# Kernel tuning notes

Hardware: AMD Instinct MI355X
Metric: run time of the kernel (lower is better)

Reference implementation:

```python
import jax, jax.numpy as jnp
import numpy as np

N_FREQS = 8
ALPHA = 16.0
SCALING = ALPHA / N_FREQS  # alpha / n_freqs
EPS = 1e-8


def setup_inputs() -> dict:
    key = jax.random.key(0)
    ks = jax.random.split(key, 6)
    B, S, IN, OUT = 4, 2048, 4096, 4096
    x = jax.random.normal(ks[0], (B, S, IN), dtype=jnp.float32)
    W = jax.random.normal(ks[1], (OUT, IN), dtype=jnp.float32) * 0.02
    bias = jax.random.normal(ks[2], (OUT,), dtype=jnp.float32) * 0.02
    delta_real = jax.random.normal(ks[3], (N_FREQS, N_FREQS), dtype=jnp.float32)
    delta_imag = jax.random.normal(ks[4], (N_FREQS, N_FREQS), dtype=jnp.float32)
    # m is initialized in torch as row-norm of the base weight; emulate that here
    m = jnp.linalg.norm(W, axis=1, keepdims=True)
    return {"x": x, "W": W, "bias": bias,
            "delta_real": delta_real, "delta_imag": delta_imag, "m": m}


def _dora_weight(W, delta_real, delta_imag, m):
    # full-size rfft2 of the frozen base weight (norm='ortho')
    W_fft = jnp.fft.rfft2(W, norm="ortho")            # [OUT, IN//2+1] complex
    fh, fw = delta_real.shape                          # freq_h, freq_w (low-freq corner)
    delta = jax.lax.complex(delta_real, delta_imag) * SCALING
    W_fft = W_fft.at[:fh, :fw].add(delta)              # pad-to-full + add, fused
    W_mod = jnp.fft.irfft2(W_fft, s=W.shape, norm="ortho")  # [OUT, IN] real
    # DoRA: magnitude m times unit row-direction
    norm = jnp.linalg.norm(W_mod, axis=1, keepdims=True)     # [OUT, 1]
    return m * W_mod / (norm + EPS)


def reference(x, W, bias, delta_real, delta_imag, m):
    W_dora = _dora_weight(W, delta_real, delta_imag, m)      # [OUT, IN]
    # F.linear: x @ W^T + b
    return jnp.einsum("bsi,oi->bso", x, W_dora) + bias
```

## Files before the change

### kernel.cpp

```cpp
#include <hip/hip_runtime.h>
#include <hip/hip_bf16.h>

typedef __attribute__((ext_vector_type(4))) float f32x4;
typedef __attribute__((ext_vector_type(8))) short bf16x8;

#define IN_DIM 4096
#define OUT_DIM 4096
#define MROWS 8192
#define NFREQ 8
#define TWO_PI 6.283185307179586f

#define BK 64
#define NT (IN_DIM / BK)
#define LDS_BUF 32768
#define LDS_HALF 16384
#define LDS_B_REGION 65536

__device__ __forceinline__ unsigned int f2bf(float f) {
    union { float f; unsigned int u; } a;
    a.f = f;
    unsigned int u = a.u;
    u += 0x7fffu + ((u >> 16) & 1u);
    return u >> 16;
}

#define ROT_C 0.9999988234517019f
#define ROT_S 0.0015339801862847655f

__global__ __launch_bounds__(256) void prep_kernel(
    const float* __restrict__ x,
    const float* __restrict__ W,
    const float* __restrict__ dre,
    const float* __restrict__ dimg,
    const float* __restrict__ mrow,
    unsigned short* __restrict__ Wd,
    unsigned short* __restrict__ xb)
{
    const int t = threadIdx.x;

    if (blockIdx.x >= OUT_DIM) {
        const size_t idx = (size_t)(blockIdx.x - OUT_DIM) * 256 + t;
        const f32x4* p = (const f32x4*)(x + idx * 8);
        const f32x4 a = p[0], b = p[1];
        uint4 o;
        o.x = f2bf(a[0]) | (f2bf(a[1]) << 16);
        o.y = f2bf(a[2]) | (f2bf(a[3]) << 16);
        o.z = f2bf(b[0]) | (f2bf(b[1]) << 16);
        o.w = f2bf(b[2]) | (f2bf(b[3]) << 16);
        *(uint4*)(xb + idx * 8) = o;
        return;
    }

    const int o = blockIdx.x;

    float P[NFREQ], Q[NFREQ];
#pragma unroll
    for (int w = 0; w < NFREQ; ++w) { P[w] = 0.f; Q[w] = 0.f; }
#pragma unroll
    for (int h = 0; h < NFREQ; ++h) {
        const float th = (TWO_PI / 4096.0f) * (float)((h * o) & 4095);
        const float sh = __sinf(th), ch = __cosf(th);
#pragma unroll
        for (int w = 0; w < NFREQ; ++w) {
            const float A = 2.0f * dre[h * NFREQ + w];
            const float B = 2.0f * dimg[h * NFREQ + w];
            P[w] += A * ch - B * sh;
            Q[w] += A * sh + B * ch;
        }
    }
#pragma unroll
    for (int w = 0; w < NFREQ; ++w) {
        const float c = (w == 0 ? 1.0f : 2.0f) * (1.0f / 4096.0f);
        P[w] *= c; Q[w] *= c;
    }

    const int i0 = t * 16;
    const f32x4* wrow = (const f32x4*)(W + (size_t)o * IN_DIM + i0);
    float vals[16];
    float ss = 0.0f;

    const float beta0 = (TWO_PI / 4096.0f) * (float)i0;
    float cb = __cosf(beta0), sb = __sinf(beta0);

#pragma unroll
    for (int q = 0; q < 4; ++q) {
        const f32x4 wv = wrow[q];
#pragma unroll
        for (int j = 0; j < 4; ++j) {
            float cw = cb, sw = sb;
            float d = P[0] + P[1] * cw - Q[1] * sw;
#pragma unroll
            for (int w = 2; w < NFREQ; ++w) {
                const float cn = cw * cb - sw * sb;
                sw = sw * cb + cw * sb;
                cw = cn;
                d += P[w] * cw - Q[w] * sw;
            }
            const float v = wv[j] + d;
            vals[q * 4 + j] = v;
            ss += v * v;
            const float cbn = cb * ROT_C - sb * ROT_S;
            sb = sb * ROT_C + cb * ROT_S;
            cb = cbn;
        }
    }

#pragma unroll
    for (int off = 32; off > 0; off >>= 1)
        ss += __shfl_down(ss, off, 64);
    __shared__ float red[4];
    if ((t & 63) == 0) red[t >> 6] = ss;
    __syncthreads();
    const float n2 = red[0] + red[1] + red[2] + red[3];
    const float scale = mrow[o] / (sqrtf(n2) + 1e-8f);

    unsigned int wds[8];
#pragma unroll
    for (int k = 0; k < 8; ++k)
        wds[k] = f2bf(vals[2 * k] * scale) | (f2bf(vals[2 * k + 1] * scale) << 16);
    uint4* dst = (uint4*)(Wd + (size_t)o * IN_DIM + i0);
    dst[0] = make_uint4(wds[0], wds[1], wds[2], wds[3]);
    dst[1] = make_uint4(wds[4], wds[5], wds[6], wds[7]);
}


#define GLOAD(src, ldsoff)                                                    \
    __builtin_amdgcn_global_load_lds(                                         \
        (const __attribute__((address_space(1))) void*)(src),                 \
        (__attribute__((address_space(3))) void*)(smem + (ldsoff)), 16, 0, 0)

#define SBAR      asm volatile("s_barrier" ::: "memory")
#define WAITLGKM0 asm volatile("s_waitcnt lgkmcnt(0)" ::: "memory")

__device__ __forceinline__ void mfma16(
    f32x4 (&acc)[8][4], const bf16x8 (&af)[4][2], const bf16x8 (&bf)[2][2],
    int MH, int NH)
{
#pragma unroll
    for (int ks = 0; ks < 2; ++ks)
#pragma unroll
        for (int mf = 0; mf < 4; ++mf)
#pragma unroll
            for (int nf = 0; nf < 2; ++nf)
                acc[MH * 4 + mf][NH * 2 + nf] =
                    __builtin_amdgcn_mfma_f32_16x16x32_bf16(
                        af[mf][ks], bf[nf][ks], acc[MH * 4 + mf][NH * 2 + nf],
                        0, 0, 0);
}

__global__ __launch_bounds__(512, 1) void gemm8_kernel(
    const unsigned short* __restrict__ Xb,
    const unsigned short* __restrict__ Wd,
    const float* __restrict__ bias,
    float* __restrict__ out)
{
    __shared__ __align__(1024) unsigned char smem[131072];

    const int tid = threadIdx.x;
    const int wid = tid >> 6, lane = tid & 63;
    const int wr = wid >> 2, wc = wid & 3;
    const int fr = lane & 15, fq = lane >> 4;

    const int bid = blockIdx.x;
    const int xcd = bid & 7;
    const int u = bid >> 3;
    const int tm = u >> 1;
    const int tn = 2 * xcd + (u & 1);
    const int m0 = tm * 256, n0 = tn * 256;

    const int srr = wid * 16 + (lane >> 3);
    const int scc = ((lane & 7) ^ (lane >> 3)) * 8;
    const unsigned short* aS = Xb + (size_t)(m0 + srr) * IN_DIM + scc;
    const unsigned short* bS = Wd + (size_t)(n0 + srr) * IN_DIM + scc;
    const int sdst = wid * 2048;

    const int cbyte = ((fq ^ (fr & 7)) * 16);
    const int aBase0 = (wr * 128 + fr) * 128 + cbyte;
    const int aBase1 = aBase0 ^ 64;
    const int bBase0 = LDS_B_REGION + (wc * 64 + fr) * 128 + cbyte;
    const int bBase1 = bBase0 ^ 64;

    auto STAGE = [&](int buf, int isB, int half, int tt) {
        const unsigned short* s =
            (isB ? bS : aS) + (size_t)half * 128 * IN_DIM + (size_t)tt * BK;
        const int d = buf * LDS_BUF + isB * LDS_B_REGION + half * LDS_HALF + sdst;
        GLOAD(s, d);
        GLOAD(s + 8 * IN_DIM, d + 1024);
    };

    f32x4 acc[8][4] = {};
    bf16x8 a0[4][2], a1[4][2], bb[2][2];

    STAGE(0, 0, 0, 0); STAGE(0, 0, 1, 0);
    STAGE(0, 1, 0, 0); STAGE(0, 1, 1, 0);
    STAGE(1, 0, 0, 1); STAGE(1, 0, 1, 1);
    STAGE(1, 1, 0, 1);
    asm volatile("s_waitcnt vmcnt(6)" ::: "memory");
    SBAR;

    for (int t = 0; t < NT; ++t) {
        const int b = t & 1;
        const int bo = b * LDS_BUF;
        const bool st1 = (t + 1 < NT);
        const bool st2 = (t + 2 < NT);

#pragma unroll
        for (int mf = 0; mf < 4; ++mf) {
            a0[mf][0] = *(const bf16x8*)(smem + bo + aBase0 + mf * 2048);
            a0[mf][1] = *(const bf16x8*)(smem + bo + aBase1 + mf * 2048);
        }
#pragma unroll
        for (int nf = 0; nf < 2; ++nf) {
            bb[nf][0] = *(const bf16x8*)(smem + bo + bBase0 + nf * 2048);
            bb[nf][1] = *(const bf16x8*)(smem + bo + bBase1 + nf * 2048);
        }
        if (st1) STAGE(b ^ 1, 1, 1, t + 1);
        __builtin_amdgcn_s_setprio(1);
        mfma16(acc, a0, bb, 0, 0);
        __builtin_amdgcn_s_setprio(0);

#pragma unroll
        for (int mf = 0; mf < 4; ++mf) {
            a1[mf][0] = *(const bf16x8*)(smem + bo + aBase0 + 8192 + mf * 2048);
            a1[mf][1] = *(const bf16x8*)(smem + bo + aBase1 + 8192 + mf * 2048);
        }
        __builtin_amdgcn_s_setprio(1);
        mfma16(acc, a1, bb, 1, 0);
        __builtin_amdgcn_s_setprio(0);
        WAITLGKM0;
        SBAR;

#pragma unroll
        for (int nf = 0; nf < 2; ++nf) {
            bb[nf][0] = *(const bf16x8*)(smem + bo + bBase0 + 4096 + nf * 2048);
            bb[nf][1] = *(const bf16x8*)(smem + bo + bBase1 + 4096 + nf * 2048);
        }
        if (st2) STAGE(b, 0, 0, t + 2);
        __builtin_amdgcn_s_setprio(1);
        mfma16(acc, a1, bb, 1, 1);
        __builtin_amdgcn_s_setprio(0);
        WAITLGKM0;
        SBAR;

        if (st2) { STAGE(b, 0, 1, t + 2); STAGE(b, 1, 0, t + 2); }
        __builtin_amdgcn_s_setprio(1);
        mfma16(acc, a0, bb, 0, 1);
        __builtin_amdgcn_s_setprio(0);
        if (st2) {
            asm volatile("s_waitcnt vmcnt(6)" ::: "memory");
        } else {
            asm volatile("s_waitcnt vmcnt(0)" ::: "memory");
        }
        SBAR;
    }

#pragma unroll
    for (int nf = 0; nf < 4; ++nf) {
        const int col = n0 + wc * 64 + nf * 16 + fr;
        const float bv = bias[col];
#pragma unroll
        for (int mf = 0; mf < 8; ++mf) {
            const int row = m0 + wr * 128 + mf * 16 + fq * 4;
            float* op = out + (size_t)row * OUT_DIM + col;
            op[0 * OUT_DIM] = acc[mf][nf][0] + bv;
            op[1 * OUT_DIM] = acc[mf][nf][1] + bv;
            op[2 * OUT_DIM] = acc[mf][nf][2] + bv;
            op[3 * OUT_DIM] = acc[mf][nf][3] + bv;
        }
    }
}

__global__ __launch_bounds__(256) void gemm_fallback(
    const float* __restrict__ Xf,
    const unsigned short* __restrict__ Wd,
    const float* __restrict__ bias,
    float* __restrict__ out)
{
    __shared__ unsigned short As[2][128 * 32];
    __shared__ unsigned short Bs[2][128 * 32];

    const int t = threadIdx.x;
    const int wid = t >> 6, lane = t & 63;
    const int wr = wid >> 1, wc = wid & 1;
    const int m0 = blockIdx.x * 128, n0 = blockIdx.y * 128;
    const int fr = lane & 15, fq = lane >> 4;

    f32x4 acc[4][4] = {};

    const int srow = wid * 16 + (lane >> 2);
    const int scol = (lane & 3) * 8;
    const unsigned short* bsrc0 = Wd + (size_t)(n0 + srow) * IN_DIM + scol;
    const unsigned short* bsrc1 = bsrc0 + (size_t)64 * IN_DIM;
    const int lds_off = wid * 512;

    const int ar = t >> 1;
    const int ak = (t & 1) * 16;
    const float* afp = Xf + (size_t)(m0 + ar) * IN_DIM + ak;
    const int a_lds_off = ar * 32 + ak;

    auto stageB = [&](unsigned short* ldsbase, int kt) {
        __builtin_amdgcn_global_load_lds(
            (const __attribute__((address_space(1))) void*)(bsrc0 + kt * 32),
            (__attribute__((address_space(3))) void*)(ldsbase + lds_off), 16, 0, 0);
        __builtin_amdgcn_global_load_lds(
            (const __attribute__((address_space(1))) void*)(bsrc1 + kt * 32),
            (__attribute__((address_space(3))) void*)(ldsbase + 2048 + lds_off), 16, 0, 0);
    };
    auto writeA = [&](int buf, const f32x4* v) {
        unsigned int w[8];
#pragma unroll
        for (int k = 0; k < 4; ++k) {
            w[2 * k]     = f2bf(v[k][0]) | (f2bf(v[k][1]) << 16);
            w[2 * k + 1] = f2bf(v[k][2]) | (f2bf(v[k][3]) << 16);
        }
        uint4* d = (uint4*)(&As[buf][a_lds_off]);
        d[0] = make_uint4(w[0], w[1], w[2], w[3]);
        d[1] = make_uint4(w[4], w[5], w[6], w[7]);
    };

    stageB(Bs[0], 0);
    {
        f32x4 av[4];
        const f32x4* ap = (const f32x4*)afp;
        av[0] = ap[0]; av[1] = ap[1]; av[2] = ap[2]; av[3] = ap[3];
        writeA(0, av);
    }
    __syncthreads();

    for (int kt = 0; kt < IN_DIM / 32; ++kt) {
        const int cur = kt & 1;
        const bool more = (kt + 1 < IN_DIM / 32);
        f32x4 nv[4];
        if (more) {
            const f32x4* ap = (const f32x4*)(afp + (size_t)(kt + 1) * 32);
            nv[0] = ap[0]; nv[1] = ap[1]; nv[2] = ap[2]; nv[3] = ap[3];
            stageB(Bs[cur ^ 1], kt + 1);
        }
        bf16x8 afrag[4], bfrag[4];
#pragma unroll
        for (int mf = 0; mf < 4; ++mf)
            afrag[mf] = *(const bf16x8*)(&As[cur][(wr * 64 + mf * 16 + fr) * 32 + fq * 8]);
#pragma unroll
        for (int nf = 0; nf < 4; ++nf)
            bfrag[nf] = *(const bf16x8*)(&Bs[cur][(wc * 64 + nf * 16 + fr) * 32 + fq * 8]);
#pragma unroll
        for (int mf = 0; mf < 4; ++mf)
#pragma unroll
            for (int nf = 0; nf < 4; ++nf)
                acc[mf][nf] = __builtin_amdgcn_mfma_f32_16x16x32_bf16(
                    afrag[mf], bfrag[nf], acc[mf][nf], 0, 0, 0);
        if (more) writeA(cur ^ 1, nv);
        __syncthreads();
    }

#pragma unroll
    for (int nf = 0; nf < 4; ++nf) {
        const int col = n0 + wc * 64 + nf * 16 + fr;
        const float bv = bias[col];
#pragma unroll
        for (int mf = 0; mf < 4; ++mf) {
            const int row = m0 + wr * 64 + mf * 16 + fq * 4;
            float* op = out + (size_t)row * OUT_DIM + col;
            op[0 * OUT_DIM] = acc[mf][nf][0] + bv;
            op[1 * OUT_DIM] = acc[mf][nf][1] + bv;
            op[2 * OUT_DIM] = acc[mf][nf][2] + bv;
            op[3 * OUT_DIM] = acc[mf][nf][3] + bv;
        }
    }
}

extern "C" void kernel_launch(void* const* d_in, const int* in_sizes, int n_in,
                              void* d_out, int out_size, void* d_ws, size_t ws_size,
                              hipStream_t stream) {
    const float* x    = (const float*)d_in[0];
    const float* W    = (const float*)d_in[1];
    const float* bias = (const float*)d_in[2];
    const float* dre  = (const float*)d_in[3];
    const float* dimg = (const float*)d_in[4];
    const float* mrow = (const float*)d_in[5];
    float* out = (float*)d_out;

    unsigned short* Wd = (unsigned short*)d_ws;
    const size_t WD_BYTES = (size_t)OUT_DIM * IN_DIM * 2;
    const size_t XB_BYTES = (size_t)MROWS * IN_DIM * 2;
    unsigned short* Xb = (unsigned short*)((char*)d_ws + WD_BYTES);
    const bool fast = ws_size >= WD_BYTES + XB_BYTES;

    if (fast) {
        const int cvt_blocks = (MROWS * (size_t)IN_DIM / 8) / 256;
        prep_kernel<<<OUT_DIM + cvt_blocks, 256, 0, stream>>>(
            x, W, dre, dimg, mrow, Wd, Xb);
        gemm8_kernel<<<dim3((MROWS / 256) * (OUT_DIM / 256)), dim3(512), 0, stream>>>(
            Xb, Wd, bias, out);
    } else {
        prep_kernel<<<OUT_DIM, 256, 0, stream>>>(x, W, dre, dimg, mrow, Wd, Wd);
        dim3 grid(MROWS / 128, OUT_DIM / 128);
        gemm_fallback<<<grid, dim3(256), 0, stream>>>(x, Wd, bias, out);
    }
}
```

Baseline: 289.7 us.

## Use 4 waves per GEMM block with 128x128 per-wave tiles

```diff
diff --git a/kernel.cpp b/kernel.cpp
--- a/kernel.cpp
+++ b/kernel.cpp
@@ -132,23 +132,7 @@
 #define SBAR      asm volatile("s_barrier" ::: "memory")
 #define WAITLGKM0 asm volatile("s_waitcnt lgkmcnt(0)" ::: "memory")
 
-__device__ __forceinline__ void mfma16(
-    f32x4 (&acc)[8][4], const bf16x8 (&af)[4][2], const bf16x8 (&bf)[2][2],
-    int MH, int NH)
-{
-#pragma unroll
-    for (int ks = 0; ks < 2; ++ks)
-#pragma unroll
-        for (int mf = 0; mf < 4; ++mf)
-#pragma unroll
-            for (int nf = 0; nf < 2; ++nf)
-                acc[MH * 4 + mf][NH * 2 + nf] =
-                    __builtin_amdgcn_mfma_f32_16x16x32_bf16(
-                        af[mf][ks], bf[nf][ks], acc[MH * 4 + mf][NH * 2 + nf],
-                        0, 0, 0);
-}
-
-__global__ __launch_bounds__(512, 1) void gemm8_kernel(
+__global__ __launch_bounds__(256, 1) void gemm8_kernel(
     const unsigned short* __restrict__ Xb,
     const unsigned short* __restrict__ Wd,
     const float* __restrict__ bias,
@@ -158,7 +142,7 @@
 
     const int tid = threadIdx.x;
     const int wid = tid >> 6, lane = tid & 63;
-    const int wr = wid >> 2, wc = wid & 3;
+    const int wr = wid >> 1, wc = wid & 1;
     const int fr = lane & 15, fq = lane >> 4;
 
     const int bid = blockIdx.x;
@@ -168,34 +152,35 @@
     const int tn = 2 * xcd + (u & 1);
     const int m0 = tm * 256, n0 = tn * 256;
 
-    const int srr = wid * 16 + (lane >> 3);
-    const int scc = ((lane & 7) ^ (lane >> 3)) * 8;
+    const int srr = wid * 32 + (lane >> 3);
+    const int scc = ((lane & 7) ^ ((lane >> 3) & 7)) * 8;
     const unsigned short* aS = Xb + (size_t)(m0 + srr) * IN_DIM + scc;
     const unsigned short* bS = Wd + (size_t)(n0 + srr) * IN_DIM + scc;
-    const int sdst = wid * 2048;
+    const int sdst = wid * 4096;
 
     const int cbyte = ((fq ^ (fr & 7)) * 16);
     const int aBase0 = (wr * 128 + fr) * 128 + cbyte;
     const int aBase1 = aBase0 ^ 64;
-    const int bBase0 = LDS_B_REGION + (wc * 64 + fr) * 128 + cbyte;
+    const int bBase0 = LDS_B_REGION + (wc * 128 + fr) * 128 + cbyte;
     const int bBase1 = bBase0 ^ 64;
 
     auto STAGE = [&](int buf, int isB, int half, int tt) {
         const unsigned short* s =
             (isB ? bS : aS) + (size_t)half * 128 * IN_DIM + (size_t)tt * BK;
         const int d = buf * LDS_BUF + isB * LDS_B_REGION + half * LDS_HALF + sdst;
-        GLOAD(s, d);
-        GLOAD(s + 8 * IN_DIM, d + 1024);
+#pragma unroll
+        for (int j = 0; j < 4; ++j)
+            GLOAD(s + (size_t)j * 8 * IN_DIM, d + j * 1024);
     };
 
-    f32x4 acc[8][4] = {};
-    bf16x8 a0[4][2], a1[4][2], bb[2][2];
+    f32x4 acc[8][8] = {};
+    bf16x8 a0[4][2], a1[4][2], bb[4][2];
 
     STAGE(0, 0, 0, 0); STAGE(0, 0, 1, 0);
     STAGE(0, 1, 0, 0); STAGE(0, 1, 1, 0);
     STAGE(1, 0, 0, 1); STAGE(1, 0, 1, 1);
     STAGE(1, 1, 0, 1);
-    asm volatile("s_waitcnt vmcnt(6)" ::: "memory");
+    asm volatile("s_waitcnt vmcnt(12)" ::: "memory");
     SBAR;
 
     for (int t = 0; t < NT; ++t) {
@@ -210,13 +195,20 @@
             a0[mf][1] = *(const bf16x8*)(smem + bo + aBase1 + mf * 2048);
         }
 #pragma unroll
-        for (int nf = 0; nf < 2; ++nf) {
+        for (int nf = 0; nf < 4; ++nf) {
             bb[nf][0] = *(const bf16x8*)(smem + bo + bBase0 + nf * 2048);
             bb[nf][1] = *(const bf16x8*)(smem + bo + bBase1 + nf * 2048);
         }
         if (st1) STAGE(b ^ 1, 1, 1, t + 1);
         __builtin_amdgcn_s_setprio(1);
-        mfma16(acc, a0, bb, 0, 0);
+#pragma unroll
+        for (int ks = 0; ks < 2; ++ks)
+#pragma unroll
+            for (int mf = 0; mf < 4; ++mf)
+#pragma unroll
+                for (int nf = 0; nf < 4; ++nf)
+                    acc[mf][nf] = __builtin_amdgcn_mfma_f32_16x16x32_bf16(
+                        a0[mf][ks], bb[nf][ks], acc[mf][nf], 0, 0, 0);
         __builtin_amdgcn_s_setprio(0);
 
 #pragma unroll
@@ -225,29 +217,50 @@
             a1[mf][1] = *(const bf16x8*)(smem + bo + aBase1 + 8192 + mf * 2048);
         }
         __builtin_amdgcn_s_setprio(1);
-        mfma16(acc, a1, bb, 1, 0);
+#pragma unroll
+        for (int ks = 0; ks < 2; ++ks)
+#pragma unroll
+            for (int mf = 0; mf < 4; ++mf)
+#pragma unroll
+                for (int nf = 0; nf < 4; ++nf)
+                    acc[4 + mf][nf] = __builtin_amdgcn_mfma_f32_16x16x32_bf16(
+                        a1[mf][ks], bb[nf][ks], acc[4 + mf][nf], 0, 0, 0);
         __builtin_amdgcn_s_setprio(0);
         WAITLGKM0;
         SBAR;
 
 #pragma unroll
-        for (int nf = 0; nf < 2; ++nf) {
-            bb[nf][0] = *(const bf16x8*)(smem + bo + bBase0 + 4096 + nf * 2048);
-            bb[nf][1] = *(const bf16x8*)(smem + bo + bBase1 + 4096 + nf * 2048);
+        for (int nf = 0; nf < 4; ++nf) {
+            bb[nf][0] = *(const bf16x8*)(smem + bo + bBase0 + 8192 + nf * 2048);
+            bb[nf][1] = *(const bf16x8*)(smem + bo + bBase1 + 8192 + nf * 2048);
         }
         if (st2) STAGE(b, 0, 0, t + 2);
         __builtin_amdgcn_s_setprio(1);
-        mfma16(acc, a1, bb, 1, 1);
+#pragma unroll
+        for (int ks = 0; ks < 2; ++ks)
+#pragma unroll
+            for (int mf = 0; mf < 4; ++mf)
+#pragma unroll
+                for (int nf = 0; nf < 4; ++nf)
+                    acc[4 + mf][4 + nf] = __builtin_amdgcn_mfma_f32_16x16x32_bf16(
+                        a1[mf][ks], bb[nf][ks], acc[4 + mf][4 + nf], 0, 0, 0);
         __builtin_amdgcn_s_setprio(0);
         WAITLGKM0;
         SBAR;
 
         if (st2) { STAGE(b, 0, 1, t + 2); STAGE(b, 1, 0, t + 2); }
         __builtin_amdgcn_s_setprio(1);
-        mfma16(acc, a0, bb, 0, 1);
+#pragma unroll
+        for (int ks = 0; ks < 2; ++ks)
+#pragma unroll
+            for (int mf = 0; mf < 4; ++mf)
+#pragma unroll
+                for (int nf = 0; nf < 4; ++nf)
+                    acc[mf][4 + nf] = __builtin_amdgcn_mfma_f32_16x16x32_bf16(
+                        a0[mf][ks], bb[nf][ks], acc[mf][4 + nf], 0, 0, 0);
         __builtin_amdgcn_s_setprio(0);
         if (st2) {
-            asm volatile("s_waitcnt vmcnt(6)" ::: "memory");
+            asm volatile("s_waitcnt vmcnt(12)" ::: "memory");
         } else {
             asm volatile("s_waitcnt vmcnt(0)" ::: "memory");
         }
@@ -255,8 +268,8 @@
     }
 
 #pragma unroll
-    for (int nf = 0; nf < 4; ++nf) {
-        const int col = n0 + wc * 64 + nf * 16 + fr;
+    for (int nf = 0; nf < 8; ++nf) {
+        const int col = n0 + wc * 128 + nf * 16 + fr;
         const float bv = bias[col];
 #pragma unroll
         for (int mf = 0; mf < 8; ++mf) {
@@ -390,7 +403,7 @@
         const int cvt_blocks = (MROWS * (size_t)IN_DIM / 8) / 256;
         prep_kernel<<<OUT_DIM + cvt_blocks, 256, 0, stream>>>(
             x, W, dre, dimg, mrow, Wd, Xb);
-        gemm8_kernel<<<dim3((MROWS / 256) * (OUT_DIM / 256)), dim3(512), 0, stream>>>(
+        gemm8_kernel<<<dim3((MROWS / 256) * (OUT_DIM / 256)), dim3(256), 0, stream>>>(
             Xb, Wd, bias, out);
     } else {
         prep_kernel<<<OUT_DIM, 256, 0, stream>>>(x, W, dre, dimg, mrow, Wd, Wd);
```

Result: slower. 354.7 us (+22.5%).

## Fuse fp32-to-bf16 conversion of x into GEMM A-tile loading

Applied to the files above, without the earlier changes.

```diff
diff --git a/kernel.cpp b/kernel.cpp
--- a/kernel.cpp
+++ b/kernel.cpp
@@ -28,29 +28,13 @@
 #define ROT_S 0.0015339801862847655f
 
 __global__ __launch_bounds__(256) void prep_kernel(
-    const float* __restrict__ x,
     const float* __restrict__ W,
     const float* __restrict__ dre,
     const float* __restrict__ dimg,
     const float* __restrict__ mrow,
-    unsigned short* __restrict__ Wd,
-    unsigned short* __restrict__ xb)
+    unsigned short* __restrict__ Wd)
 {
     const int t = threadIdx.x;
-
-    if (blockIdx.x >= OUT_DIM) {
-        const size_t idx = (size_t)(blockIdx.x - OUT_DIM) * 256 + t;
-        const f32x4* p = (const f32x4*)(x + idx * 8);
-        const f32x4 a = p[0], b = p[1];
-        uint4 o;
-        o.x = f2bf(a[0]) | (f2bf(a[1]) << 16);
-        o.y = f2bf(a[2]) | (f2bf(a[3]) << 16);
-        o.z = f2bf(b[0]) | (f2bf(b[1]) << 16);
-        o.w = f2bf(b[2]) | (f2bf(b[3]) << 16);
-        *(uint4*)(xb + idx * 8) = o;
-        return;
-    }
-
     const int o = blockIdx.x;
 
     float P[NFREQ], Q[NFREQ];
@@ -149,7 +133,7 @@
 }
 
 __global__ __launch_bounds__(512, 1) void gemm8_kernel(
-    const unsigned short* __restrict__ Xb,
+    const float* __restrict__ x,
     const unsigned short* __restrict__ Wd,
     const float* __restrict__ bias,
     float* __restrict__ out)
@@ -170,9 +154,12 @@
 
     const int srr = wid * 16 + (lane >> 3);
     const int scc = ((lane & 7) ^ (lane >> 3)) * 8;
-    const unsigned short* aS = Xb + (size_t)(m0 + srr) * IN_DIM + scc;
     const unsigned short* bS = Wd + (size_t)(n0 + srr) * IN_DIM + scc;
     const int sdst = wid * 2048;
+
+    const int arow = wid * 16 + (lane >> 3);
+    const float* aX = x + (size_t)(m0 + arow) * IN_DIM + (lane & 7) * 8;
+    const int awb = arow * 128 + (((lane & 7) ^ ((lane >> 3) & 7)) * 16);
 
     const int cbyte = ((fq ^ (fr & 7)) * 16);
     const int aBase0 = (wr * 128 + fr) * 128 + cbyte;
@@ -180,22 +167,43 @@
     const int bBase0 = LDS_B_REGION + (wc * 64 + fr) * 128 + cbyte;
     const int bBase1 = bBase0 ^ 64;
 
-    auto STAGE = [&](int buf, int isB, int half, int tt) {
-        const unsigned short* s =
-            (isB ? bS : aS) + (size_t)half * 128 * IN_DIM + (size_t)tt * BK;
-        const int d = buf * LDS_BUF + isB * LDS_B_REGION + half * LDS_HALF + sdst;
+    auto STAGEB = [&](int buf, int half, int tt) {
+        const unsigned short* s = bS + (size_t)half * 128 * IN_DIM + (size_t)tt * BK;
+        const int d = buf * LDS_BUF + LDS_B_REGION + half * LDS_HALF + sdst;
         GLOAD(s, d);
         GLOAD(s + 8 * IN_DIM, d + 1024);
     };
+    auto ALOAD = [&](f32x4* v, int half, int j, int tt) {
+        const float* p = aX + ((size_t)half * 128 + j) * IN_DIM + (size_t)tt * BK;
+        v[0] = *(const f32x4*)(p);
+        v[1] = *(const f32x4*)(p + 4);
+    };
+    auto AWRITE = [&](int buf, int half, int j, const f32x4* v) {
+        uint4 w;
+        w.x = f2bf(v[0][0]) | (f2bf(v[0][1]) << 16);
+        w.y = f2bf(v[0][2]) | (f2bf(v[0][3]) << 16);
+        w.z = f2bf(v[1][0]) | (f2bf(v[1][1]) << 16);
+        w.w = f2bf(v[1][2]) | (f2bf(v[1][3]) << 16);
+        *(uint4*)(smem + buf * LDS_BUF + half * LDS_HALF + awb + j * 128) = w;
+    };
 
     f32x4 acc[8][4] = {};
     bf16x8 a0[4][2], a1[4][2], bb[2][2];
-
-    STAGE(0, 0, 0, 0); STAGE(0, 0, 1, 0);
-    STAGE(0, 1, 0, 0); STAGE(0, 1, 1, 0);
-    STAGE(1, 0, 0, 1); STAGE(1, 0, 1, 1);
-    STAGE(1, 1, 0, 1);
-    asm volatile("s_waitcnt vmcnt(6)" ::: "memory");
+    f32x4 av[2][2][2];
+
+    ALOAD(av[0][0], 0, 0, 0); ALOAD(av[0][1], 0, 8, 0);
+    ALOAD(av[1][0], 1, 0, 0); ALOAD(av[1][1], 1, 8, 0);
+    STAGEB(0, 0, 0); STAGEB(0, 1, 0);
+    asm volatile("s_waitcnt vmcnt(4)" ::: "memory");
+    AWRITE(0, 0, 0, av[0][0]); AWRITE(0, 0, 8, av[0][1]);
+    AWRITE(0, 1, 0, av[1][0]); AWRITE(0, 1, 8, av[1][1]);
+    ALOAD(av[0][0], 0, 0, 1); ALOAD(av[0][1], 0, 8, 1);
+    ALOAD(av[1][0], 1, 0, 1); ALOAD(av[1][1], 1, 8, 1);
+    STAGEB(1, 0, 1);
+    asm volatile("s_waitcnt vmcnt(2)" ::: "memory");
+    AWRITE(1, 0, 0, av[0][0]); AWRITE(1, 0, 8, av[0][1]);
+    AWRITE(1, 1, 0, av[1][0]); AWRITE(1, 1, 8, av[1][1]);
+    WAITLGKM0;
     SBAR;
 
     for (int t = 0; t < NT; ++t) {
@@ -214,7 +222,11 @@
             bb[nf][0] = *(const bf16x8*)(smem + bo + bBase0 + nf * 2048);
             bb[nf][1] = *(const bf16x8*)(smem + bo + bBase1 + nf * 2048);
         }
-        if (st1) STAGE(b ^ 1, 1, 1, t + 1);
+        if (st2) {
+            ALOAD(av[0][0], 0, 0, t + 2); ALOAD(av[0][1], 0, 8, t + 2);
+            ALOAD(av[1][0], 1, 0, t + 2); ALOAD(av[1][1], 1, 8, t + 2);
+        }
+        if (st1) STAGEB(b ^ 1, 1, t + 1);
         __builtin_amdgcn_s_setprio(1);
         mfma16(acc, a0, bb, 0, 0);
         __builtin_amdgcn_s_setprio(0);
@@ -235,22 +247,29 @@
             bb[nf][0] = *(const bf16x8*)(smem + bo + bBase0 + 4096 + nf * 2048);
             bb[nf][1] = *(const bf16x8*)(smem + bo + bBase1 + 4096 + nf * 2048);
         }
-        if (st2) STAGE(b, 0, 0, t + 2);
+        if (st2) {
+            asm volatile("s_waitcnt vmcnt(2)" ::: "memory");
+            AWRITE(b, 0, 0, av[0][0]); AWRITE(b, 0, 8, av[0][1]);
+        }
         __builtin_amdgcn_s_setprio(1);
         mfma16(acc, a1, bb, 1, 1);
         __builtin_amdgcn_s_setprio(0);
         WAITLGKM0;
         SBAR;
 
-        if (st2) { STAGE(b, 0, 1, t + 2); STAGE(b, 1, 0, t + 2); }
+        if (st2) {
+            AWRITE(b, 1, 0, av[1][0]); AWRITE(b, 1, 8, av[1][1]);
+            STAGEB(b, 0, t + 2);
+        }
         __builtin_amdgcn_s_setprio(1);
         mfma16(acc, a0, bb, 0, 1);
         __builtin_amdgcn_s_setprio(0);
         if (st2) {
-            asm volatile("s_waitcnt vmcnt(6)" ::: "memory");
+            asm volatile("s_waitcnt vmcnt(2)" ::: "memory");
         } else {
             asm volatile("s_waitcnt vmcnt(0)" ::: "memory");
         }
+        WAITLGKM0;
         SBAR;
     }
 
@@ -382,18 +401,14 @@
 
     unsigned short* Wd = (unsigned short*)d_ws;
     const size_t WD_BYTES = (size_t)OUT_DIM * IN_DIM * 2;
-    const size_t XB_BYTES = (size_t)MROWS * IN_DIM * 2;
-    unsigned short* Xb = (unsigned short*)((char*)d_ws + WD_BYTES);
-    const bool fast = ws_size >= WD_BYTES + XB_BYTES;
+    const bool fast = ws_size >= WD_BYTES;
+
+    prep_kernel<<<OUT_DIM, 256, 0, stream>>>(W, dre, dimg, mrow, Wd);
 
     if (fast) {
-        const int cvt_blocks = (MROWS * (size_t)IN_DIM / 8) / 256;
-        prep_kernel<<<OUT_DIM + cvt_blocks, 256, 0, stream>>>(
-            x, W, dre, dimg, mrow, Wd, Xb);
         gemm8_kernel<<<dim3((MROWS / 256) * (OUT_DIM / 256)), dim3(512), 0, stream>>>(
-            Xb, Wd, bias, out);
+            x, Wd, bias, out);
     } else {
-        prep_kernel<<<OUT_DIM, 256, 0, stream>>>(x, W, dre, dimg, mrow, Wd, Wd);
         dim3 grid(MROWS / 128, OUT_DIM / 128);
         gemm_fallback<<<grid, dim3(256), 0, stream>>>(x, Wd, bias, out);
     }
```

New measurement: 474.7 us. 1.64x slower.
